# Kernel optimization log

Hardware: AMD Instinct MI355X
Metric: run time of the kernel (lower is better)

## Reference

```python
import jax, jax.numpy as jnp
import numpy as np

N = 100000   # nodes
E = 1600000  # directed edges (avg degree 16)
H = 64       # MODEL_HIDDEN_CHANNELS


def setup_inputs() -> dict:
    key = jax.random.key(0)
    ks = jax.random.split(key, 6)
    x = jax.random.normal(ks[0], (N, 1), dtype=jnp.float32)
    edge_index = jax.random.randint(ks[1], (2, E), 0, N, dtype=jnp.int32)
    w1 = jax.random.normal(ks[2], (1, H), dtype=jnp.float32) * 0.5
    b1 = jnp.zeros((H,), dtype=jnp.float32)
    w2 = jax.random.normal(ks[3], (H, H), dtype=jnp.float32) * (1.0 / np.sqrt(H))
    b2 = jnp.zeros((H,), dtype=jnp.float32)
    wfc = jax.random.normal(ks[4], (H, 1), dtype=jnp.float32) * (1.0 / np.sqrt(H))
    bfc = jnp.zeros((1,), dtype=jnp.float32)
    return {"x": x, "edge_index": edge_index, "w1": w1, "b1": b1,
            "w2": w2, "b2": b2, "wfc": wfc, "bfc": bfc}


def _gcn_conv(x, src, dst, norm, W, b, n):
    # PyG GCNConv: h = x @ W, then scatter-add of norm-weighted messages at dst, + bias
    h = x @ W                                   # [n, out]
    msg = h[src] * norm[:, None]                # gather + scale, [e, out]
    agg = jax.ops.segment_sum(msg, dst, num_segments=n)
    return agg + b


def reference(x, edge_index, w1, b1, w2, b2, wfc, bfc):
    n = x.shape[0]
    # add self-loops (PyG GCNConv default)
    loops = jnp.arange(n, dtype=edge_index.dtype)
    src = jnp.concatenate([edge_index[0], loops])
    dst = jnp.concatenate([edge_index[1], loops])
    # symmetric degree normalization D^{-1/2} A_hat D^{-1/2}
    deg = jax.ops.segment_sum(jnp.ones(src.shape[0], dtype=x.dtype), dst, num_segments=n)
    dinv = jnp.where(deg > 0, jax.lax.rsqrt(deg), 0.0)
    norm = dinv[src] * dinv[dst]
    h = jax.nn.relu(_gcn_conv(x, src, dst, norm, w1, b1, n))
    h = jax.nn.relu(_gcn_conv(h, src, dst, norm, w2, b2, n))
    out = h @ wfc + bfc                         # [n, 1]
    return out.reshape(-1)
```

## Files before the change

kernel.cpp:

```cpp
#include <hip/hip_runtime.h>


#define HCH 64
#define CHUNK 4096
#define BSH 7
#define BSZ 128
#define NBMAX 1024

__device__ __forceinline__ void lds_addf(float* p, float v) {
    __hip_atomic_fetch_add(p, v, __ATOMIC_RELAXED, __HIP_MEMORY_SCOPE_WORKGROUP);
}

__global__ __launch_bounds__(512) void k_place(const int* __restrict__ src,
                                               const int* __restrict__ dst, int e,
                                               int nb, int cap,
                                               int* __restrict__ cursorRel,
                                               int* __restrict__ ov_cursor,
                                               int* __restrict__ packed,
                                               int2* __restrict__ ovbuf) {
    __shared__ int h[NBMAX];
    __shared__ int scanE[NBMAX];
    __shared__ int basel[NBMAX];
    __shared__ int avail[NBMAX];
    __shared__ int slpv[CHUNK];
    __shared__ short ssb[CHUNK];
    __shared__ int wsum[8];
    int t = threadIdx.x;
    for (int i = t; i < NBMAX; i += 512) h[i] = 0;
    __syncthreads();
    int cbase = blockIdx.x * CHUNK;
    int rem = min(e - cbase, CHUNK);
    int li = t * 8;
    bool fast = (li + 7 < rem);

    int4 sA, sB, dA, dB;
    if (fast) {
        sA = *(const int4*)(src + cbase + li);
        sB = *(const int4*)(src + cbase + li + 4);
        dA = *(const int4*)(dst + cbase + li);
        dB = *(const int4*)(dst + cbase + li + 4);
        atomicAdd(&h[dA.x >> BSH], 1); atomicAdd(&h[dA.y >> BSH], 1);
        atomicAdd(&h[dA.z >> BSH], 1); atomicAdd(&h[dA.w >> BSH], 1);
        atomicAdd(&h[dB.x >> BSH], 1); atomicAdd(&h[dB.y >> BSH], 1);
        atomicAdd(&h[dB.z >> BSH], 1); atomicAdd(&h[dB.w >> BSH], 1);
    } else {
        for (int q = li; q < rem && q < li + 8; q++)
            atomicAdd(&h[dst[cbase + q] >> BSH], 1);
    }
    __syncthreads();

    int v0 = h[2 * t], v1 = h[2 * t + 1];
    for (int i = t; i < nb; i += 512) {
        int my = h[i];
        int av = 0, base = 0;
        if (my) {
            int baseRel = atomicAdd(&cursorRel[i], my);
            base = i * cap + baseRel;
            int room = cap - baseRel;
            av = room < 0 ? 0 : (room > my ? my : room);
        }
        basel[i] = base;
        avail[i] = av;
    }
    int lane = t & 63, wid = t >> 6;
    int s = v0 + v1;
    int incl = s;
#pragma unroll
    for (int d = 1; d < 64; d <<= 1) {
        int o = __shfl_up(incl, d, 64);
        if (lane >= d) incl += o;
    }
    if (lane == 63) wsum[wid] = incl;
    __syncthreads();
    if (t < 8) {
        int v = wsum[t];
        int inc2 = v;
#pragma unroll
        for (int d = 1; d < 8; d <<= 1) {
            int o = __shfl_up(inc2, d, 8);
            if (t >= d) inc2 += o;
        }
        wsum[t] = inc2 - v;
    }
    for (int i = t; i < NBMAX; i += 512) h[i] = 0;
    __syncthreads();
    int excl = incl - s + wsum[wid];
    scanE[2 * t] = excl;
    scanE[2 * t + 1] = excl + v0;
    __syncthreads();

    if (fast) {
#pragma unroll
        for (int q = 0; q < 8; q++) {
            int sv = (q == 0) ? sA.x : (q == 1) ? sA.y : (q == 2) ? sA.z :
                     (q == 3) ? sA.w : (q == 4) ? sB.x : (q == 5) ? sB.y :
                     (q == 6) ? sB.z : sB.w;
            int dv = (q == 0) ? dA.x : (q == 1) ? dA.y : (q == 2) ? dA.z :
                     (q == 3) ? dA.w : (q == 4) ? dB.x : (q == 5) ? dB.y :
                     (q == 6) ? dB.z : dB.w;
            int b = dv >> BSH;
            int pos = scanE[b] + atomicAdd(&h[b], 1);
            slpv[pos] = sv | ((dv & (BSZ - 1)) << 17);
            ssb[pos] = (short)b;
        }
    } else {
        for (int q = li; q < rem && q < li + 8; q++) {
            int sv = src[cbase + q], dv = dst[cbase + q];
            int b = dv >> BSH;
            int pos = scanE[b] + atomicAdd(&h[b], 1);
            slpv[pos] = sv | ((dv & (BSZ - 1)) << 17);
            ssb[pos] = (short)b;
        }
    }
    __syncthreads();

    for (int jj = t; jj < rem; jj += 512) {
        int b = ssb[jj];
        int loc = jj - scanE[b];
        int pv = slpv[jj];
        if (loc < avail[b]) {
            packed[basel[b] + loc] = pv;
        } else {
            int op = atomicAdd(ov_cursor, 1);
            ovbuf[op] = make_int2(pv & 0x1FFFF, (b << BSH) | (pv >> 17));
        }
    }
}

__global__ __launch_bounds__(512) void k_bdeg(const int* __restrict__ packed,
                                              const int* __restrict__ cursorRel,
                                              const int* __restrict__ ov_cursor,
                                              const int2* __restrict__ ovbuf,
                                              int cap, const float* __restrict__ x, int n,
                                              float* __restrict__ dinv,
                                              float* __restrict__ y) {
    __shared__ int cnt[BSZ];
    int bk = blockIdx.x, t = threadIdx.x;
    int bbase = bk * cap;
    int bcnt = min(cursorRel[bk], cap);
    if (t < BSZ) cnt[t] = 0;
    __syncthreads();
    for (int base = 0; base < bcnt; base += 2048) {
        int i0 = base + t * 4;
        if (i0 + 3 < bcnt) {
            int4 p = *(const int4*)(packed + bbase + i0);
            atomicAdd(&cnt[p.x >> 17], 1);
            atomicAdd(&cnt[p.y >> 17], 1);
            atomicAdd(&cnt[p.z >> 17], 1);
            atomicAdd(&cnt[p.w >> 17], 1);
        } else {
            for (int i = i0; i < bcnt && i < i0 + 4; i++)
                atomicAdd(&cnt[packed[bbase + i] >> 17], 1);
        }
    }
    int ovc = *ov_cursor;
    for (int i = t; i < ovc; i += 512) {
        int2 o = ovbuf[i];
        if ((o.y >> BSH) == bk) atomicAdd(&cnt[o.y & (BSZ - 1)], 1);
    }
    __syncthreads();
    int node = (bk << BSH) + t;
    if (t < BSZ && node < n) {
        float dv = rsqrtf((float)(cnt[t] + 1));
        dinv[node] = dv;
        y[node] = dv * x[node];
    }
}

__global__ __launch_bounds__(512) void k_bagg1(const int* __restrict__ packed,
                                               const int* __restrict__ cursorRel,
                                               const int* __restrict__ ov_cursor,
                                               const int2* __restrict__ ovbuf,
                                               int cap,
                                               const float* __restrict__ dinv,
                                               const float* __restrict__ y, int n,
                                               float2* __restrict__ val2) {
    __shared__ float acc[BSZ];
    int bk = blockIdx.x, t = threadIdx.x;
    int bbase = bk * cap;
    int bcnt = min(cursorRel[bk], cap);
    if (t < BSZ) acc[t] = 0.f;
    __syncthreads();
    for (int base = 0; base < bcnt; base += 2048) {
        int i0 = base + t * 4;
        if (i0 + 3 < bcnt) {
            int4 p = *(const int4*)(packed + bbase + i0);
            float y0 = y[p.x & 0x1FFFF], y1 = y[p.y & 0x1FFFF];
            float y2 = y[p.z & 0x1FFFF], y3 = y[p.w & 0x1FFFF];
            lds_addf(&acc[p.x >> 17], y0);
            lds_addf(&acc[p.y >> 17], y1);
            lds_addf(&acc[p.z >> 17], y2);
            lds_addf(&acc[p.w >> 17], y3);
        } else {
            for (int i = i0; i < bcnt && i < i0 + 4; i++) {
                int p = packed[bbase + i];
                lds_addf(&acc[p >> 17], y[p & 0x1FFFF]);
            }
        }
    }
    int ovc = *ov_cursor;
    for (int i = t; i < ovc; i += 512) {
        int2 o = ovbuf[i];
        if ((o.y >> BSH) == bk) lds_addf(&acc[o.y & (BSZ - 1)], y[o.x]);
    }
    __syncthreads();
    int node = (bk << BSH) + t;
    if (t < BSZ && node < n) {
        float dv = dinv[node];
        float s = dv * (acc[t] + y[node]);
        val2[node] = make_float2(dv * s, dv);
    }
}

__global__ __launch_bounds__(512) void k_bagg2(const int* __restrict__ packed,
                                               const int* __restrict__ cursorRel,
                                               const int* __restrict__ ov_cursor,
                                               const int2* __restrict__ ovbuf,
                                               int cap, const float2* __restrict__ val2,
                                               const float* __restrict__ dinv,
                                               const float* __restrict__ w1,
                                               const float* __restrict__ b1,
                                               const float* __restrict__ w2,
                                               const float* __restrict__ b2,
                                               const float* __restrict__ wfc,
                                               const float* __restrict__ bfc,
                                               float* __restrict__ out, int n) {
    __shared__ float aa[2 * BSZ];
    __shared__ float cc[2 * BSZ];
    __shared__ float part[8][4][HCH];
    __shared__ float sP[4 * HCH], sb2[HCH], swfc[HCH];
    __shared__ float part2[4][BSZ];
    __shared__ float fsum;
    int bk = blockIdx.x, t = threadIdx.x;
    int bbase = bk * cap;
    int bcnt = min(cursorRel[bk], cap);

    {
        int j = t & 63, seg = t >> 6;
        float pp = 0.f, pm = 0.f, bp = 0.f, bm = 0.f;
#pragma unroll
        for (int kk = 0; kk < 8; kk++) {
            int k = seg * 8 + kk;
            float w = w1[k], b = b1[k], v = w2[k * HCH + j];
            if (w > 0.f) { pp += w * v; bp += b * v; }
            else if (w < 0.f) { pm += w * v; bm += b * v; }
            else { float rb = b > 0.f ? b : 0.f; bp += rb * v; bm += rb * v; }
        }
        part[seg][0][j] = pp; part[seg][1][j] = pm;
        part[seg][2][j] = bp; part[seg][3][j] = bm;
    }
    if (t < 256) aa[t] = 0.f; else cc[t - 256] = 0.f;
    if (t >= 256 && t < 320) sb2[t - 256] = b2[t - 256];
    if (t >= 320 && t < 384) swfc[t - 320] = wfc[t - 320];
    if (t == 448) fsum = 0.f;
    __syncthreads();
    if (t < 4 * HCH) {
        int c = t >> 6, jj = t & 63;
        float ssum = 0.f;
#pragma unroll
        for (int g = 0; g < 8; g++) ssum += part[g][c][jj];
        sP[t] = ssum;
        if (c >= 2) lds_addf(&fsum, fabsf(ssum));
    }
    __syncthreads();
    bool useB = fsum != 0.f;

    for (int base = 0; base < bcnt; base += 2048) {
        int i0 = base + t * 4;
        if (i0 + 3 < bcnt) {
            int4 p = *(const int4*)(packed + bbase + i0);
            float2 v0 = val2[p.x & 0x1FFFF], v1 = val2[p.y & 0x1FFFF];
            float2 v2 = val2[p.z & 0x1FFFF], v3 = val2[p.w & 0x1FFFF];
            int o0 = (v0.x > 0.f ? 0 : BSZ) + (p.x >> 17);
            int o1 = (v1.x > 0.f ? 0 : BSZ) + (p.y >> 17);
            int o2 = (v2.x > 0.f ? 0 : BSZ) + (p.z >> 17);
            int o3 = (v3.x > 0.f ? 0 : BSZ) + (p.w >> 17);
            lds_addf(&aa[o0], v0.x); lds_addf(&aa[o1], v1.x);
            lds_addf(&aa[o2], v2.x); lds_addf(&aa[o3], v3.x);
            if (useB) {
                lds_addf(&cc[o0], v0.y); lds_addf(&cc[o1], v1.y);
                lds_addf(&cc[o2], v2.y); lds_addf(&cc[o3], v3.y);
            }
        } else {
            for (int i = i0; i < bcnt && i < i0 + 4; i++) {
                int p = packed[bbase + i];
                float2 v = val2[p & 0x1FFFF];
                int off = (v.x > 0.f ? 0 : BSZ) + (p >> 17);
                lds_addf(&aa[off], v.x);
                if (useB) lds_addf(&cc[off], v.y);
            }
        }
    }
    int ovc = *ov_cursor;
    for (int i = t; i < ovc; i += 512) {
        int2 o = ovbuf[i];
        if ((o.y >> BSH) == bk) {
            float2 v = val2[o.x];
            int off = (v.x > 0.f ? 0 : BSZ) + (o.y & (BSZ - 1));
            lds_addf(&aa[off], v.x);
            if (useB) lds_addf(&cc[off], v.y);
        }
    }
    __syncthreads();

    int tt = t & (BSZ - 1), q = t >> 7;
    int node = (bk << BSH) + tt;
    if (node < n) {
        float a_p = aa[tt], a_m = aa[BSZ + tt];
        float c_p = cc[tt], c_m = cc[BSZ + tt];
        float2 sv = val2[node];
        if (sv.x > 0.f) { a_p += sv.x; c_p += sv.y; }
        else            { a_m += sv.x; c_m += sv.y; }
        float dv = dinv[node];
        float pacc = 0.f;
#pragma unroll
        for (int u = 0; u < 16; u++) {
            int j = q * 16 + u;
            float z = dv * (a_p * sP[j] + a_m * sP[HCH + j] +
                            c_p * sP[2 * HCH + j] + c_m * sP[3 * HCH + j]) + sb2[j];
            z = z > 0.f ? z : 0.f;
            pacc += z * swfc[j];
        }
        part2[q][tt] = pacc;
    }
    __syncthreads();
    if (t < BSZ) {
        int nd = (bk << BSH) + t;
        if (nd < n)
            out[nd] = part2[0][t] + part2[1][t] + part2[2][t] + part2[3][t] + bfc[0];
    }
}

extern "C" void kernel_launch(void* const* d_in, const int* in_sizes, int n_in,
                              void* d_out, int out_size, void* d_ws, size_t ws_size,
                              hipStream_t stream) {
    const float* x   = (const float*)d_in[0];
    const int*   ei  = (const int*)d_in[1];
    const float* w1  = (const float*)d_in[2];
    const float* b1  = (const float*)d_in[3];
    const float* w2  = (const float*)d_in[4];
    const float* b2  = (const float*)d_in[5];
    const float* wfc = (const float*)d_in[6];
    const float* bfc = (const float*)d_in[7];
    float* out = (float*)d_out;

    const int n = in_sizes[0];
    const int e = in_sizes[1] / 2;
    const int* src = ei;
    const int* dst = ei + e;

    const int nb = (n + BSZ - 1) >> BSH;
    int avg = (e + nb - 1) / nb;
    int cap = ((avg + avg / 4 + 64) + 15) & ~15;

    auto al = [](size_t v) { return (v + 255) & ~(size_t)255; };
    char* ws = (char*)d_ws;
    size_t o = 0;
    int* cursorRel = (int*)(ws + o);  o = al(o + (size_t)NBMAX * 4);
    int* ov_cursor = (int*)(ws + o);  o = al(o + 256);
    float* dinv  = (float*)(ws + o);  o = al(o + (size_t)n * 4);
    float* y     = (float*)(ws + o);  o = al(o + (size_t)n * 4);
    float2* val2 = (float2*)(ws + o); o = al(o + (size_t)n * 8);
    int* packed  = (int*)(ws + o);    o = al(o + (size_t)nb * cap * 4);
    int2* ovbuf  = (int2*)(ws + o);   o = al(o + (size_t)e * 8);
    (void)ws_size;

    const int nchunk = (e + CHUNK - 1) / CHUNK;

    hipMemsetAsync(ws, 0, (size_t)NBMAX * 4 + 4, stream);
    k_place<<<nchunk, 512, 0, stream>>>(src, dst, e, nb, cap, cursorRel, ov_cursor,
                                        packed, ovbuf);
    k_bdeg<<<nb, 512, 0, stream>>>(packed, cursorRel, ov_cursor, ovbuf, cap, x, n,
                                   dinv, y);
    k_bagg1<<<nb, 512, 0, stream>>>(packed, cursorRel, ov_cursor, ovbuf, cap, dinv, y,
                                    n, val2);
    k_bagg2<<<nb, 512, 0, stream>>>(packed, cursorRel, ov_cursor, ovbuf, cap, val2,
                                    dinv, w1, b1, w2, b2, wfc, bfc, out, n);
}
```

Baseline: 134.3 us.

## Double place chunk size and split val2 into separate val and dinv gathers

The placement kernel now handles 8192 edges per block instead of 4096, looping in int4 strides, and re-reads src/dst in the second pass rather than keeping them in registers. This halves the number of blocks and their global cursor atomics, and puts longer contiguous runs per bucket into the packed writes. The float2 val2 array becomes a plain float val. The second aggregation now gathers the dinv value separately, only when useB is set, so the common path loads 4 bytes per edge instead of 8. The cost is an extra random gather from dinv when useB is active, and larger LDS staging (slpv/ssb) per block in k_place, which lowers occupancy.

Result: no change. 133.9 us (-0.3%).

```diff
diff --git a/kernel.cpp b/kernel.cpp
--- a/kernel.cpp
+++ b/kernel.cpp
@@ -2,7 +2,7 @@
 
 
 #define HCH 64
-#define CHUNK 4096
+#define CHUNK 8192
 #define BSH 7
 #define BSZ 128
 #define NBMAX 1024
@@ -30,22 +30,20 @@
     __syncthreads();
     int cbase = blockIdx.x * CHUNK;
     int rem = min(e - cbase, CHUNK);
-    int li = t * 8;
-    bool fast = (li + 7 < rem);
-
-    int4 sA, sB, dA, dB;
-    if (fast) {
-        sA = *(const int4*)(src + cbase + li);
-        sB = *(const int4*)(src + cbase + li + 4);
-        dA = *(const int4*)(dst + cbase + li);
-        dB = *(const int4*)(dst + cbase + li + 4);
-        atomicAdd(&h[dA.x >> BSH], 1); atomicAdd(&h[dA.y >> BSH], 1);
-        atomicAdd(&h[dA.z >> BSH], 1); atomicAdd(&h[dA.w >> BSH], 1);
-        atomicAdd(&h[dB.x >> BSH], 1); atomicAdd(&h[dB.y >> BSH], 1);
-        atomicAdd(&h[dB.z >> BSH], 1); atomicAdd(&h[dB.w >> BSH], 1);
-    } else {
-        for (int q = li; q < rem && q < li + 8; q++)
-            atomicAdd(&h[dst[cbase + q] >> BSH], 1);
+
+#pragma unroll
+    for (int k = 0; k < CHUNK / 2048; k++) {
+        int li = (k * 512 + t) * 4;
+        if (li + 3 < rem) {
+            int4 d4 = *(const int4*)(dst + cbase + li);
+            atomicAdd(&h[d4.x >> BSH], 1);
+            atomicAdd(&h[d4.y >> BSH], 1);
+            atomicAdd(&h[d4.z >> BSH], 1);
+            atomicAdd(&h[d4.w >> BSH], 1);
+        } else {
+            for (int q = li; q < rem && q < li + 4; q++)
+                atomicAdd(&h[dst[cbase + q] >> BSH], 1);
+        }
     }
     __syncthreads();
 
@@ -89,27 +87,29 @@
     scanE[2 * t + 1] = excl + v0;
     __syncthreads();
 
-    if (fast) {
-#pragma unroll
-        for (int q = 0; q < 8; q++) {
-            int sv = (q == 0) ? sA.x : (q == 1) ? sA.y : (q == 2) ? sA.z :
-                     (q == 3) ? sA.w : (q == 4) ? sB.x : (q == 5) ? sB.y :
-                     (q == 6) ? sB.z : sB.w;
-            int dv = (q == 0) ? dA.x : (q == 1) ? dA.y : (q == 2) ? dA.z :
-                     (q == 3) ? dA.w : (q == 4) ? dB.x : (q == 5) ? dB.y :
-                     (q == 6) ? dB.z : dB.w;
-            int b = dv >> BSH;
-            int pos = scanE[b] + atomicAdd(&h[b], 1);
-            slpv[pos] = sv | ((dv & (BSZ - 1)) << 17);
-            ssb[pos] = (short)b;
-        }
-    } else {
-        for (int q = li; q < rem && q < li + 8; q++) {
-            int sv = src[cbase + q], dv = dst[cbase + q];
-            int b = dv >> BSH;
-            int pos = scanE[b] + atomicAdd(&h[b], 1);
-            slpv[pos] = sv | ((dv & (BSZ - 1)) << 17);
-            ssb[pos] = (short)b;
+#pragma unroll
+    for (int k = 0; k < CHUNK / 2048; k++) {
+        int li = (k * 512 + t) * 4;
+        if (li + 3 < rem) {
+            int4 s4 = *(const int4*)(src + cbase + li);
+            int4 d4 = *(const int4*)(dst + cbase + li);
+#pragma unroll
+            for (int q = 0; q < 4; q++) {
+                int sv = (q == 0) ? s4.x : (q == 1) ? s4.y : (q == 2) ? s4.z : s4.w;
+                int dv = (q == 0) ? d4.x : (q == 1) ? d4.y : (q == 2) ? d4.z : d4.w;
+                int b = dv >> BSH;
+                int pos = scanE[b] + atomicAdd(&h[b], 1);
+                slpv[pos] = sv | ((dv & (BSZ - 1)) << 17);
+                ssb[pos] = (short)b;
+            }
+        } else {
+            for (int q = li; q < rem && q < li + 4; q++) {
+                int sv = src[cbase + q], dv = dst[cbase + q];
+                int b = dv >> BSH;
+                int pos = scanE[b] + atomicAdd(&h[b], 1);
+                slpv[pos] = sv | ((dv & (BSZ - 1)) << 17);
+                ssb[pos] = (short)b;
+            }
         }
     }
     __syncthreads();
@@ -174,7 +174,7 @@
                                                int cap,
                                                const float* __restrict__ dinv,
                                                const float* __restrict__ y, int n,
-                                               float2* __restrict__ val2) {
+                                               float* __restrict__ val) {
     __shared__ float acc[BSZ];
     int bk = blockIdx.x, t = threadIdx.x;
     int bbase = bk * cap;
@@ -208,7 +208,7 @@
     if (t < BSZ && node < n) {
         float dv = dinv[node];
         float s = dv * (acc[t] + y[node]);
-        val2[node] = make_float2(dv * s, dv);
+        val[node] = dv * s;
     }
 }
 
@@ -216,7 +216,7 @@
                                                const int* __restrict__ cursorRel,
                                                const int* __restrict__ ov_cursor,
                                                const int2* __restrict__ ovbuf,
-                                               int cap, const float2* __restrict__ val2,
+                                               int cap, const float* __restrict__ val,
                                                const float* __restrict__ dinv,
                                                const float* __restrict__ w1,
                                                const float* __restrict__ b1,
@@ -269,25 +269,27 @@
         int i0 = base + t * 4;
         if (i0 + 3 < bcnt) {
             int4 p = *(const int4*)(packed + bbase + i0);
-            float2 v0 = val2[p.x & 0x1FFFF], v1 = val2[p.y & 0x1FFFF];
-            float2 v2 = val2[p.z & 0x1FFFF], v3 = val2[p.w & 0x1FFFF];
-            int o0 = (v0.x > 0.f ? 0 : BSZ) + (p.x >> 17);
-            int o1 = (v1.x > 0.f ? 0 : BSZ) + (p.y >> 17);
-            int o2 = (v2.x > 0.f ? 0 : BSZ) + (p.z >> 17);
-            int o3 = (v3.x > 0.f ? 0 : BSZ) + (p.w >> 17);
-            lds_addf(&aa[o0], v0.x); lds_addf(&aa[o1], v1.x);
-            lds_addf(&aa[o2], v2.x); lds_addf(&aa[o3], v3.x);
+            float v0 = val[p.x & 0x1FFFF], v1 = val[p.y & 0x1FFFF];
+            float v2 = val[p.z & 0x1FFFF], v3 = val[p.w & 0x1FFFF];
+            int o0 = (v0 > 0.f ? 0 : BSZ) + (p.x >> 17);
+            int o1 = (v1 > 0.f ? 0 : BSZ) + (p.y >> 17);
+            int o2 = (v2 > 0.f ? 0 : BSZ) + (p.z >> 17);
+            int o3 = (v3 > 0.f ? 0 : BSZ) + (p.w >> 17);
+            lds_addf(&aa[o0], v0); lds_addf(&aa[o1], v1);
+            lds_addf(&aa[o2], v2); lds_addf(&aa[o3], v3);
             if (useB) {
-                lds_addf(&cc[o0], v0.y); lds_addf(&cc[o1], v1.y);
-                lds_addf(&cc[o2], v2.y); lds_addf(&cc[o3], v3.y);
+                lds_addf(&cc[o0], dinv[p.x & 0x1FFFF]);
+                lds_addf(&cc[o1], dinv[p.y & 0x1FFFF]);
+                lds_addf(&cc[o2], dinv[p.z & 0x1FFFF]);
+                lds_addf(&cc[o3], dinv[p.w & 0x1FFFF]);
             }
         } else {
             for (int i = i0; i < bcnt && i < i0 + 4; i++) {
                 int p = packed[bbase + i];
-                float2 v = val2[p & 0x1FFFF];
-                int off = (v.x > 0.f ? 0 : BSZ) + (p >> 17);
-                lds_addf(&aa[off], v.x);
-                if (useB) lds_addf(&cc[off], v.y);
+                float v = val[p & 0x1FFFF];
+                int off = (v > 0.f ? 0 : BSZ) + (p >> 17);
+                lds_addf(&aa[off], v);
+                if (useB) lds_addf(&cc[off], dinv[p & 0x1FFFF]);
             }
         }
     }
@@ -295,10 +297,10 @@
     for (int i = t; i < ovc; i += 512) {
         int2 o = ovbuf[i];
         if ((o.y >> BSH) == bk) {
-            float2 v = val2[o.x];
-            int off = (v.x > 0.f ? 0 : BSZ) + (o.y & (BSZ - 1));
-            lds_addf(&aa[off], v.x);
-            if (useB) lds_addf(&cc[off], v.y);
+            float v = val[o.x];
+            int off = (v > 0.f ? 0 : BSZ) + (o.y & (BSZ - 1));
+            lds_addf(&aa[off], v);
+            if (useB) lds_addf(&cc[off], dinv[o.x]);
         }
     }
     __syncthreads();
@@ -308,10 +310,10 @@
     if (node < n) {
         float a_p = aa[tt], a_m = aa[BSZ + tt];
         float c_p = cc[tt], c_m = cc[BSZ + tt];
-        float2 sv = val2[node];
-        if (sv.x > 0.f) { a_p += sv.x; c_p += sv.y; }
-        else            { a_m += sv.x; c_m += sv.y; }
         float dv = dinv[node];
+        float sx = val[node];
+        if (sx > 0.f) { a_p += sx; c_p += dv; }
+        else          { a_m += sx; c_m += dv; }
         float pacc = 0.f;
 #pragma unroll
         for (int u = 0; u < 16; u++) {
@@ -360,7 +362,7 @@
     int* ov_cursor = (int*)(ws + o);  o = al(o + 256);
     float* dinv  = (float*)(ws + o);  o = al(o + (size_t)n * 4);
     float* y     = (float*)(ws + o);  o = al(o + (size_t)n * 4);
-    float2* val2 = (float2*)(ws + o); o = al(o + (size_t)n * 8);
+    float* val   = (float*)(ws + o);  o = al(o + (size_t)n * 4);
     int* packed  = (int*)(ws + o);    o = al(o + (size_t)nb * cap * 4);
     int2* ovbuf  = (int2*)(ws + o);   o = al(o + (size_t)e * 8);
     (void)ws_size;
@@ -373,7 +375,7 @@
     k_bdeg<<<nb, 512, 0, stream>>>(packed, cursorRel, ov_cursor, ovbuf, cap, x, n,
                                    dinv, y);
     k_bagg1<<<nb, 512, 0, stream>>>(packed, cursorRel, ov_cursor, ovbuf, cap, dinv, y,
-                                    n, val2);
-    k_bagg2<<<nb, 512, 0, stream>>>(packed, cursorRel, ov_cursor, ovbuf, cap, val2,
+                                    n, val);
+    k_bagg2<<<nb, 512, 0, stream>>>(packed, cursorRel, ov_cursor, ovbuf, cap, val,
                                     dinv, w1, b1, w2, b2, wfc, bfc, out, n);
 }
```
